# Kernel optimization log

Measured on AMD Instinct MI355X. Metric: run time of the kernel, lower is better.

The kernel has to match this reference:

```python
import jax, jax.numpy as jnp
import numpy as np

D = 128          # feature / hidden dim
K = 3            # SortPooling k (hard-coded in Topkpool)
NUM_CLASS = 10
EPS = 1e-5       # BatchNorm eps


def setup_inputs() -> dict:
    key = jax.random.key(0)
    ks = jax.random.split(key, 24)
    G, NPG = 512, 200
    N = G * NPG
    E = 1638400
    inp = {
        "x": jax.random.normal(ks[0], (N, D), jnp.float32),
        "src": jax.random.randint(ks[1], (E,), 0, N),
        "dst": jax.random.randint(ks[2], (E,), 0, N),
        "num_graphs": G,
        "nodes_per_graph": NPG,
    }
    s = 1.0 / np.sqrt(D)
    for i in (1, 2, 3):
        inp[f"W{i}"] = jax.random.uniform(ks[2 + i], (D, D), jnp.float32, -s, s)
        inp[f"b{i}"] = jnp.zeros((D,), jnp.float32)
        inp[f"g{i}"] = jnp.ones((D,), jnp.float32)   # BN gamma
        inp[f"bt{i}"] = jnp.zeros((D,), jnp.float32)  # BN beta
    sp = 1.0 / np.sqrt(K * D)
    for i in range(4):
        inp[f"P{i}w"] = jax.random.uniform(ks[10 + i], (K * D, NUM_CLASS), jnp.float32, -sp, sp)
        inp[f"P{i}b"] = jnp.zeros((NUM_CLASS,), jnp.float32)
    return inp


def _graph_conv(h, src, dst, W, b, n):
    # DGL GraphConv, norm='both': D_in^{-1/2} A (D_out^{-1/2} h) W + b
    one = jnp.ones((src.shape[0],), h.dtype)
    deg_out = jnp.zeros((n,), h.dtype).at[src].add(one)
    deg_in = jnp.zeros((n,), h.dtype).at[dst].add(one)
    h = h * jax.lax.rsqrt(jnp.maximum(deg_out, 1.0))[:, None]
    agg = jax.ops.segment_sum(h[src], dst, num_segments=n)  # [N, D] scatter-add
    agg = agg * jax.lax.rsqrt(jnp.maximum(deg_in, 1.0))[:, None]
    return agg @ W + b


def _bn_relu(h, g, bt):
    mu = h.mean(axis=0)
    var = jnp.mean((h - mu) ** 2, axis=0)  # biased var, torch BN training mode
    return jax.nn.relu((h - mu) * jax.lax.rsqrt(var + EPS) * g + bt)


def _sort_pool(h, G, npg):
    # DGL SortPooling: sort each node's feature vector ascending, then pick
    # top-K nodes per graph by last (max) channel, concatenate features.
    d = h.shape[-1]
    hs = jnp.sort(h, axis=-1).reshape(G, npg, d)
    idx = jax.lax.top_k(hs[:, :, -1], K)[1]                       # [G, K]
    return jnp.take_along_axis(hs, idx[:, :, None], axis=1).reshape(G, K * d)


def reference(x, W1, b1, g1, bt1, W2, b2, g2, bt2, W3, b3, g3, bt3,
              P0w, P0b, P1w, P1b, P2w, P2b, P3w, P3b,
              src, dst, num_graphs, nodes_per_graph):
    n = x.shape[0]
    reps = [x]
    h = x
    for W, b, g, bt in ((W1, b1, g1, bt1), (W2, b2, g2, bt2), (W3, b3, g3, bt3)):
        h = _bn_relu(_graph_conv(h, src, dst, W, b, n), g, bt)
        reps.append(h)
    score = jnp.zeros((num_graphs, NUM_CLASS), x.dtype)
    for h_i, Pw, Pb in zip(reps, (P0w, P1w, P2w, P3w), (P0b, P1b, P2b, P3b)):
        score = score + _sort_pool(h_i, num_graphs, nodes_per_graph) @ Pw + Pb
    return score
```

## Files before the change

kernel.cpp:

```cpp
#include <hip/hip_runtime.h>
#include <hip/hip_bf16.h>

#define D 128
#define KTOP 3
#define NCLS 10
#define EPS 1e-5f
#define GBM 128
#define BCAP 64


__global__ __launch_bounds__(256) void prologue_kernel(
        const int* __restrict__ src,
        int* __restrict__ deg_out, int E,
        const float* __restrict__ x, float* __restrict__ nodemax, int N,
        float* __restrict__ score, const float* __restrict__ pb0,
        const float* __restrict__ pb1, const float* __restrict__ pb2,
        const float* __restrict__ pb3, int G) {
    int b = blockIdx.x;
    int nbDeg = (E + 255) >> 8;
    if (b < nbDeg) {
        int e = b * 256 + threadIdx.x;
        if (e < E) atomicAdd(&deg_out[src[e]], 1);
        return;
    }
    b -= nbDeg;
    int nbR = N >> 3;
    if (b < nbR) {
        int node = b * 8 + (threadIdx.x >> 5);
        int l = threadIdx.x & 31;
        float4 v = *reinterpret_cast<const float4*>(x + (size_t)node * D + 4 * l);
        float m = fmaxf(fmaxf(v.x, v.y), fmaxf(v.z, v.w));
#pragma unroll
        for (int d = 16; d > 0; d >>= 1) m = fmaxf(m, __shfl_xor(m, d, 64));
        if (l == 0) nodemax[node] = m;
        return;
    }
    for (int i = threadIdx.x; i < G * NCLS; i += 256) {
        int c = i % NCLS;
        score[i] = pb0[c] + pb1[c] + pb2[c] + pb3[c];
    }
}

__global__ void csr_scatter(const int* __restrict__ src, const int* __restrict__ dst,
                            const int* __restrict__ deg_out,
                            int* __restrict__ cursor, int2* __restrict__ csrw, int E) {
    int e = blockIdx.x * blockDim.x + threadIdx.x;
    if (e >= E) return;
    int d = dst[e], s = src[e];
    int slot = atomicAdd(&cursor[d], 1);
    if (slot >= BCAP) return;
    int dg = deg_out[s]; if (dg < 1) dg = 1;
    int2 p; p.x = s; p.y = __float_as_int(rsqrtf((float)dg));
    csrw[(size_t)d * BCAP + slot] = p;
}

__global__ void pad_kernel(const int* __restrict__ cursor, int2* __restrict__ csrw, int N) {
    int d = blockIdx.x * blockDim.x + threadIdx.x;
    if (d >= N) return;
    int c = cursor[d]; if (c > BCAP) c = BCAP;
    int end = (c + 7) & ~7;
    int2 z; z.x = 0; z.y = 0;
    for (int i = c; i < end; ++i) csrw[(size_t)d * BCAP + i] = z;
}

__device__ __forceinline__ float4 bnrelu4(float4 v, float4 sc, float4 sh) {
    float4 r;
    r.x = fmaxf(fmaf(v.x, sc.x, sh.x), 0.f);
    r.y = fmaxf(fmaf(v.y, sc.y, sh.y), 0.f);
    r.z = fmaxf(fmaf(v.z, sc.z, sh.z), 0.f);
    r.w = fmaxf(fmaf(v.w, sc.w, sh.w), 0.f);
    return r;
}


__global__ __launch_bounds__(256) void aggregate_head(
        const float* __restrict__ hin, const int* __restrict__ cursor,
        const int2* __restrict__ csrw, float* __restrict__ hout, int nAgg,
        const float* __restrict__ nodemax, const float* __restrict__ Pw,
        float* __restrict__ score, int NPG,
        const float* __restrict__ bns, const float* __restrict__ g,
        const float* __restrict__ bt, float invN) {
    __shared__ float ov[256];
    __shared__ float sv[256];
    __shared__ int   si[256];
    __shared__ int   sel[KTOP];
    __shared__ float sbuf[KTOP][D];
    __shared__ float red[4][NCLS];
    __shared__ float scs[D], shs[D];
    int b = blockIdx.x;
    int t = threadIdx.x;
    bool useBN = (bns != nullptr);
    if (useBN) {
        if (t < D) {
            float mu  = bns[t] * invN;
            float var = bns[D + t] * invN - mu * mu;
            float inv = rsqrtf(var + EPS);
            float s = g[t] * inv;
            scs[t] = s;
            shs[t] = bt[t] - mu * s;
        }
        __syncthreads();
    }
    if (b < nAgg) {
        int node = b * 8 + (t >> 5);
        int l = t & 31;
        int deg = cursor[node];
        int end = (deg + 7) & ~7; if (end > BCAP) end = BCAP;
        const int2* bkt = csrw + (size_t)node * BCAP;
        const float* base = hin + 4 * l;
        float4 sc4, sh4;
        if (useBN) {
            sc4 = *reinterpret_cast<const float4*>(&scs[4 * l]);
            sh4 = *reinterpret_cast<const float4*>(&shs[4 * l]);
        }
        float4 a0 = {0.f, 0.f, 0.f, 0.f}, a1 = a0;
        for (int e = 0; e < end; e += 8) {
            const int4* ce = reinterpret_cast<const int4*>(bkt + e);
            int4 p0 = ce[0], p1 = ce[1], p2 = ce[2], p3 = ce[3];
            float4 v0 = *reinterpret_cast<const float4*>(base + (size_t)p0.x * D);
            float4 v1 = *reinterpret_cast<const float4*>(base + (size_t)p0.z * D);
            float4 v2 = *reinterpret_cast<const float4*>(base + (size_t)p1.x * D);
            float4 v3 = *reinterpret_cast<const float4*>(base + (size_t)p1.z * D);
            float4 v4 = *reinterpret_cast<const float4*>(base + (size_t)p2.x * D);
            float4 v5 = *reinterpret_cast<const float4*>(base + (size_t)p2.z * D);
            float4 v6 = *reinterpret_cast<const float4*>(base + (size_t)p3.x * D);
            float4 v7 = *reinterpret_cast<const float4*>(base + (size_t)p3.z * D);
            if (useBN) {
                v0 = bnrelu4(v0, sc4, sh4); v1 = bnrelu4(v1, sc4, sh4);
                v2 = bnrelu4(v2, sc4, sh4); v3 = bnrelu4(v3, sc4, sh4);
                v4 = bnrelu4(v4, sc4, sh4); v5 = bnrelu4(v5, sc4, sh4);
                v6 = bnrelu4(v6, sc4, sh4); v7 = bnrelu4(v7, sc4, sh4);
            }
            float w0 = __int_as_float(p0.y), w1 = __int_as_float(p0.w);
            float w2 = __int_as_float(p1.y), w3 = __int_as_float(p1.w);
            float w4 = __int_as_float(p2.y), w5 = __int_as_float(p2.w);
            float w6 = __int_as_float(p3.y), w7 = __int_as_float(p3.w);
            a0.x += w0*v0.x; a0.y += w0*v0.y; a0.z += w0*v0.z; a0.w += w0*v0.w;
            a1.x += w1*v1.x; a1.y += w1*v1.y; a1.z += w1*v1.z; a1.w += w1*v1.w;
            a0.x += w2*v2.x; a0.y += w2*v2.y; a0.z += w2*v2.z; a0.w += w2*v2.w;
            a1.x += w3*v3.x; a1.y += w3*v3.y; a1.z += w3*v3.z; a1.w += w3*v3.w;
            a0.x += w4*v4.x; a0.y += w4*v4.y; a0.z += w4*v4.z; a0.w += w4*v4.w;
            a1.x += w5*v5.x; a1.y += w5*v5.y; a1.z += w5*v5.z; a1.w += w5*v5.w;
            a0.x += w6*v6.x; a0.y += w6*v6.y; a0.z += w6*v6.z; a0.w += w6*v6.w;
            a1.x += w7*v7.x; a1.y += w7*v7.y; a1.z += w7*v7.z; a1.w += w7*v7.w;
        }
        float ri = rsqrtf((float)(deg < 1 ? 1 : deg));
        float4 r;
        r.x = (a0.x + a1.x) * ri;
        r.y = (a0.y + a1.y) * ri;
        r.z = (a0.z + a1.z) * ri;
        r.w = (a0.w + a1.w) * ri;
        *reinterpret_cast<float4*>(hout + (size_t)node * D + 4 * l) = r;
        return;
    }

    int gr = b - nAgg;
    ov[t] = (t < NPG) ? nodemax[(size_t)gr * NPG + t] : -3.4e38f;
    __syncthreads();
    for (int ks = 0; ks < KTOP; ++ks) {
        sv[t] = ov[t]; si[t] = t;
        __syncthreads();
        for (int s = 128; s > 0; s >>= 1) {
            if (t < s) {
                float a = sv[t], c = sv[t + s];
                int ia = si[t], ib = si[t + s];
                if (c > a || (c == a && ib < ia)) { sv[t] = c; si[t] = ib; }
            }
            __syncthreads();
        }
        if (t == 0) { sel[ks] = si[0]; ov[si[0]] = -3.4e38f; }
        __syncthreads();
    }
    int u = t >> 7, tl = t & 127;
    {
        float v = hin[((size_t)gr * NPG + sel[u]) * D + tl];
        sbuf[u][tl] = useBN ? fmaxf(fmaf(v, scs[tl], shs[tl]), 0.f) : v;
        if (t < 128) {
            float v2 = hin[((size_t)gr * NPG + sel[2]) * D + t];
            sbuf[2][t] = useBN ? fmaxf(fmaf(v2, scs[t], shs[t]), 0.f) : v2;
        }
    }
    __syncthreads();
    for (int size = 2; size <= D; size <<= 1) {
        for (int stride = size >> 1; stride > 0; stride >>= 1) {
            int ixj = tl ^ stride;
            if (ixj > tl) {
                float a = sbuf[u][tl], c = sbuf[u][ixj];
                bool up = ((tl & size) == 0);
                if ((a > c) == up) { sbuf[u][tl] = c; sbuf[u][ixj] = a; }
            }
            if (t < 128) {
                int ix2 = t ^ stride;
                if (ix2 > t) {
                    float a = sbuf[2][t], c = sbuf[2][ix2];
                    bool up = ((t & size) == 0);
                    if ((a > c) == up) { sbuf[2][t] = c; sbuf[2][ix2] = a; }
                }
            }
            __syncthreads();
        }
    }
    float part[NCLS];
    float v0 = sbuf[u][tl];
    const float* pw0 = Pw + (size_t)(u * D + tl) * NCLS;
#pragma unroll
    for (int c = 0; c < NCLS; ++c) part[c] = v0 * pw0[c];
    if (t < 128) {
        float v2 = sbuf[2][t];
        const float* pw2 = Pw + (size_t)(2 * D + t) * NCLS;
#pragma unroll
        for (int c = 0; c < NCLS; ++c) part[c] += v2 * pw2[c];
    }
    int lane = t & 63, wid = t >> 6;
#pragma unroll
    for (int c = 0; c < NCLS; ++c) {
        float xx = part[c];
#pragma unroll
        for (int o = 32; o > 0; o >>= 1) xx += __shfl_down(xx, o, 64);
        if (lane == 0) red[wid][c] = xx;
    }
    __syncthreads();
    if (t < NCLS)
        atomicAdd(&score[gr * NCLS + t],
                  red[0][t] + red[1][t] + red[2][t] + red[3][t]);
}


__device__ __forceinline__ void gemm_chunk(const float* __restrict__ ain, size_t rowBase,
        int kc, int c0, const float (*Wl)[D], float (&acc)[4][8]) {
#pragma unroll 2
    for (int k4 = 0; k4 < 16; ++k4) {
        const float* ap = ain + rowBase * D + kc + 4 * k4;
        float4 a0 = *reinterpret_cast<const float4*>(ap);
        float4 a1 = *reinterpret_cast<const float4*>(ap + D);
        float4 a2 = *reinterpret_cast<const float4*>(ap + 2 * D);
        float4 a3 = *reinterpret_cast<const float4*>(ap + 3 * D);
#pragma unroll
        for (int j = 0; j < 4; ++j) {
            int kk = 4 * k4 + j;
            float4 w0 = *reinterpret_cast<const float4*>(&Wl[kk][c0]);
            float4 w1 = *reinterpret_cast<const float4*>(&Wl[kk][c0 + 4]);
            float av[4];
            av[0] = (j==0)?a0.x:(j==1)?a0.y:(j==2)?a0.z:a0.w;
            av[1] = (j==0)?a1.x:(j==1)?a1.y:(j==2)?a1.z:a1.w;
            av[2] = (j==0)?a2.x:(j==1)?a2.y:(j==2)?a2.z:a2.w;
            av[3] = (j==0)?a3.x:(j==1)?a3.y:(j==2)?a3.z:a3.w;
            float wv[8] = {w0.x, w0.y, w0.z, w0.w, w1.x, w1.y, w1.z, w1.w};
#pragma unroll
            for (int i = 0; i < 4; ++i)
#pragma unroll
                for (int jj = 0; jj < 8; ++jj) acc[i][jj] += av[i] * wv[jj];
        }
    }
}

__global__ __launch_bounds__(512) void gemm_bn(const float* __restrict__ ain,
        const float* __restrict__ W, const float* __restrict__ bias,
        float* __restrict__ hout, float* __restrict__ bnsums, int N) {
    __shared__ __align__(16) float Wl[64][D];
    int t = threadIdx.x;
    int cg = t & 15;
    int rs = t >> 4;
    int c0 = cg * 8;
    size_t rowBase = (size_t)blockIdx.x * GBM + 4 * rs;

    float acc[4][8];
#pragma unroll
    for (int i = 0; i < 4; ++i)
#pragma unroll
        for (int j = 0; j < 8; ++j) acc[i][j] = 0.f;

    const float4* Wv = reinterpret_cast<const float4*>(W);
    float4* Wd = reinterpret_cast<float4*>(&Wl[0][0]);
    float4 wpre[4];
#pragma unroll
    for (int i = 0; i < 4; ++i) wpre[i] = Wv[t + 512 * i];
#pragma unroll
    for (int i = 0; i < 4; ++i) Wd[t + 512 * i] = wpre[i];
#pragma unroll
    for (int i = 0; i < 4; ++i) wpre[i] = Wv[2048 + t + 512 * i];
    __syncthreads();
    gemm_chunk(ain, rowBase, 0, c0, Wl, acc);
    __syncthreads();
#pragma unroll
    for (int i = 0; i < 4; ++i) Wd[t + 512 * i] = wpre[i];
    __syncthreads();
    gemm_chunk(ain, rowBase, 64, c0, Wl, acc);

    float4 b0 = *reinterpret_cast<const float4*>(&bias[c0]);
    float4 b1 = *reinterpret_cast<const float4*>(&bias[c0 + 4]);
    float bv[8] = {b0.x, b0.y, b0.z, b0.w, b1.x, b1.y, b1.z, b1.w};
    float cs[8], cq[8];
#pragma unroll
    for (int j = 0; j < 8; ++j) { cs[j] = 0.f; cq[j] = 0.f; }
#pragma unroll
    for (int i = 0; i < 4; ++i) {
#pragma unroll
        for (int j = 0; j < 8; ++j) {
            float v = acc[i][j] + bv[j];
            acc[i][j] = v;
            cs[j] += v;
            cq[j] += v * v;
        }
    }
#pragma unroll
    for (int i = 0; i < 4; ++i) {
        size_t row = rowBase + i;
        float4 o0, o1;
        o0.x = acc[i][0]; o0.y = acc[i][1]; o0.z = acc[i][2]; o0.w = acc[i][3];
        o1.x = acc[i][4]; o1.y = acc[i][5]; o1.z = acc[i][6]; o1.w = acc[i][7];
        *reinterpret_cast<float4*>(&hout[row * D + c0])     = o0;
        *reinterpret_cast<float4*>(&hout[row * D + c0 + 4]) = o1;
    }
#pragma unroll
    for (int j = 0; j < 8; ++j) {
        cs[j] += __shfl_xor(cs[j], 16, 64); cq[j] += __shfl_xor(cq[j], 16, 64);
        cs[j] += __shfl_xor(cs[j], 32, 64); cq[j] += __shfl_xor(cq[j], 32, 64);
    }
    __syncthreads();
    float* red = &Wl[0][0];
    int wid = t >> 6, lane = t & 63;
    if (lane < 16) {
#pragma unroll
        for (int j = 0; j < 8; ++j) {
            red[wid * 256 + lane * 16 + j]     = cs[j];
            red[wid * 256 + lane * 16 + 8 + j] = cq[j];
        }
    }
    __syncthreads();
    if (t < 256) {
        float s = 0.f;
#pragma unroll
        for (int w = 0; w < 8; ++w) s += red[w * 256 + t];
        int cgi = t >> 4, r = t & 15;
        int ch = cgi * 8 + (r & 7);
        atomicAdd(&bnsums[(r < 8 ? 0 : D) + ch], s);
    }
}


__global__ __launch_bounds__(256) void bn_nodemax(const float* __restrict__ h,
        const float* __restrict__ bnsums, const float* __restrict__ g,
        const float* __restrict__ bt, float* __restrict__ nodemax, int N, float invN) {
    __shared__ float sc[D], sh[D];
    int t = threadIdx.x;
    if (t < D) {
        float mu  = bnsums[t] * invN;
        float var = bnsums[D + t] * invN - mu * mu;
        float inv = rsqrtf(var + EPS);
        float s = g[t] * inv;
        sc[t] = s;
        sh[t] = bt[t] - mu * s;
    }
    __syncthreads();
    int node = (blockIdx.x * 256 + t) >> 5;
    int l = t & 31;
    if (node >= N) return;
    float4 v = *reinterpret_cast<const float4*>(h + (size_t)node * D + 4 * l);
    float4 a = *reinterpret_cast<const float4*>(&sc[4 * l]);
    float4 b = *reinterpret_cast<const float4*>(&sh[4 * l]);
    v.x = fmaxf(fmaf(v.x, a.x, b.x), 0.f);
    v.y = fmaxf(fmaf(v.y, a.y, b.y), 0.f);
    v.z = fmaxf(fmaf(v.z, a.z, b.z), 0.f);
    v.w = fmaxf(fmaf(v.w, a.w, b.w), 0.f);
    float m = fmaxf(fmaxf(v.x, v.y), fmaxf(v.z, v.w));
#pragma unroll
    for (int d = 16; d > 0; d >>= 1) m = fmaxf(m, __shfl_xor(m, d, 64));
    if (l == 0) nodemax[node] = m;
}


extern "C" void kernel_launch(void* const* d_in, const int* in_sizes, int n_in,
                              void* d_out, int out_size, void* d_ws, size_t ws_size,
                              hipStream_t stream) {
    const float* x   = (const float*)d_in[0];
    const int*   src = (const int*)d_in[1];
    const int*   dst = (const int*)d_in[2];
    const float* W[3]  = {(const float*)d_in[5],  (const float*)d_in[9],  (const float*)d_in[13]};
    const float* bb[3] = {(const float*)d_in[6],  (const float*)d_in[10], (const float*)d_in[14]};
    const float* gg[3] = {(const float*)d_in[7],  (const float*)d_in[11], (const float*)d_in[15]};
    const float* bt[3] = {(const float*)d_in[8],  (const float*)d_in[12], (const float*)d_in[16]};
    const float* Pw[4] = {(const float*)d_in[17], (const float*)d_in[19], (const float*)d_in[21], (const float*)d_in[23]};
    const float* Pb[4] = {(const float*)d_in[18], (const float*)d_in[20], (const float*)d_in[22], (const float*)d_in[24]};

    int N = in_sizes[0] / D;
    int E = in_sizes[1];
    int G = out_size / NCLS;
    int NPG = N / G;
    float* score = (float*)d_out;

    size_t NF = (size_t)N * D;
    float* fws     = (float*)d_ws;
    float* H       = fws;
    float* T       = H + NF;
    float* nodemax = T + NF;
    float* bnsums  = nodemax + N;
    int* deg_out = (int*)(bnsums + 6 * D);
    int* cursor  = deg_out + N;
    int2* csrw   = (int2*)(cursor + N);

    int nbDeg = (E + 255) >> 8;
    int nbR = N >> 3;
    float invN = 1.0f / (float)N;

    hipMemsetAsync(deg_out, 0, sizeof(int) * (size_t)2 * N, stream);
    hipMemsetAsync(bnsums, 0, sizeof(float) * 6 * D, stream);

    prologue_kernel<<<nbDeg + nbR + 1, 256, 0, stream>>>(
        src, deg_out, E, x, nodemax, N,
        score, Pb[0], Pb[1], Pb[2], Pb[3], G);
    csr_scatter<<<(E + 255) / 256, 256, 0, stream>>>(src, dst, deg_out, cursor, csrw, E);
    pad_kernel<<<(N + 255) / 256, 256, 0, stream>>>(cursor, csrw, N);

    int nAgg = N / 8;
    const float* hin = x;
    const float* curBns = nullptr;
    const float* curG = nullptr;
    const float* curBt = nullptr;
    for (int l = 0; l < 3; ++l) {
        float* bns = bnsums + l * 2 * D;
        aggregate_head<<<nAgg + G, 256, 0, stream>>>(
            hin, cursor, csrw, T, nAgg, nodemax, Pw[l], score, NPG,
            curBns, curG, curBt, invN);
        gemm_bn<<<N / GBM, 512, 0, stream>>>(T, W[l], bb[l], H, bns, N);
        bn_nodemax<<<N / 8, 256, 0, stream>>>(H, bns, gg[l], bt[l], nodemax, N, invN);
        hin = H;
        curBns = bns; curG = gg[l]; curBt = bt[l];
    }
    aggregate_head<<<G, 256, 0, stream>>>(
        H, cursor, csrw, T, 0, nodemax, Pw[3], score, NPG,
        curBns, curG, curBt, invN);
}
```

Before: 833.7 us.

## Partition degree and CSR atomics by XCD node range; prefetch GEMM A tiles

The degree-count and CSR-scatter kernels now launch eight times as many blocks. Blocks are interleaved by XCD (blockIdx & 7), and each block only performs atomics for nodes in its XCD's slice of the node range, so atomic traffic to a given address stays within one XCD's L2. This costs eight reads of the src/dst arrays and many more blocks. Separately, the GEMM inner loop software-prefetches the next A float4 group before computing on the current one.

```diff
diff --git a/kernel.cpp b/kernel.cpp
--- a/kernel.cpp
+++ b/kernel.cpp
@@ -18,12 +18,17 @@
         const float* __restrict__ pb3, int G) {
     int b = blockIdx.x;
     int nbDeg = (E + 255) >> 8;
-    if (b < nbDeg) {
-        int e = b * 256 + threadIdx.x;
-        if (e < E) atomicAdd(&deg_out[src[e]], 1);
+    if (b < 8 * nbDeg) {
+        int xcd = b & 7;
+        int e = (b >> 3) * 256 + threadIdx.x;
+        int lo = xcd * (N >> 3), hi = lo + (N >> 3);
+        if (e < E) {
+            int s = src[e];
+            if (s >= lo && s < hi) atomicAdd(&deg_out[s], 1);
+        }
         return;
     }
-    b -= nbDeg;
+    b -= 8 * nbDeg;
     int nbR = N >> 3;
     if (b < nbR) {
         int node = b * 8 + (threadIdx.x >> 5);
@@ -41,12 +46,19 @@
     }
 }
 
-__global__ void csr_scatter(const int* __restrict__ src, const int* __restrict__ dst,
-                            const int* __restrict__ deg_out,
-                            int* __restrict__ cursor, int2* __restrict__ csrw, int E) {
-    int e = blockIdx.x * blockDim.x + threadIdx.x;
+
+__global__ __launch_bounds__(256) void csr_scatter(
+        const int* __restrict__ src, const int* __restrict__ dst,
+        const int* __restrict__ deg_out,
+        int* __restrict__ cursor, int2* __restrict__ csrw, int E, int N) {
+    int b = blockIdx.x;
+    int xcd = b & 7;
+    int e = (b >> 3) * 256 + threadIdx.x;
     if (e >= E) return;
-    int d = dst[e], s = src[e];
+    int d = dst[e];
+    int lo = xcd * (N >> 3), hi = lo + (N >> 3);
+    if (d < lo || d >= hi) return;
+    int s = src[e];
     int slot = atomicAdd(&cursor[d], 1);
     if (slot >= BCAP) return;
     int dg = deg_out[s]; if (dg < 1) dg = 1;
@@ -228,13 +240,21 @@
 
 __device__ __forceinline__ void gemm_chunk(const float* __restrict__ ain, size_t rowBase,
         int kc, int c0, const float (*Wl)[D], float (&acc)[4][8]) {
+    const float* ap = ain + rowBase * D + kc;
+    float4 a0 = *reinterpret_cast<const float4*>(ap);
+    float4 a1 = *reinterpret_cast<const float4*>(ap + D);
+    float4 a2 = *reinterpret_cast<const float4*>(ap + 2 * D);
+    float4 a3 = *reinterpret_cast<const float4*>(ap + 3 * D);
 #pragma unroll 2
     for (int k4 = 0; k4 < 16; ++k4) {
-        const float* ap = ain + rowBase * D + kc + 4 * k4;
-        float4 a0 = *reinterpret_cast<const float4*>(ap);
-        float4 a1 = *reinterpret_cast<const float4*>(ap + D);
-        float4 a2 = *reinterpret_cast<const float4*>(ap + 2 * D);
-        float4 a3 = *reinterpret_cast<const float4*>(ap + 3 * D);
+        float4 n0 = a0, n1 = a1, n2 = a2, n3 = a3;
+        if (k4 < 15) {
+            const float* np = ap + 4 * (k4 + 1);
+            n0 = *reinterpret_cast<const float4*>(np);
+            n1 = *reinterpret_cast<const float4*>(np + D);
+            n2 = *reinterpret_cast<const float4*>(np + 2 * D);
+            n3 = *reinterpret_cast<const float4*>(np + 3 * D);
+        }
 #pragma unroll
         for (int j = 0; j < 4; ++j) {
             int kk = 4 * k4 + j;
@@ -251,6 +271,7 @@
 #pragma unroll
                 for (int jj = 0; jj < 8; ++jj) acc[i][jj] += av[i] * wv[jj];
         }
+        a0 = n0; a1 = n1; a2 = n2; a3 = n3;
     }
 }
 
@@ -406,10 +427,10 @@
     hipMemsetAsync(deg_out, 0, sizeof(int) * (size_t)2 * N, stream);
     hipMemsetAsync(bnsums, 0, sizeof(float) * 6 * D, stream);
 
-    prologue_kernel<<<nbDeg + nbR + 1, 256, 0, stream>>>(
+    prologue_kernel<<<8 * nbDeg + nbR + 1, 256, 0, stream>>>(
         src, deg_out, E, x, nodemax, N,
         score, Pb[0], Pb[1], Pb[2], Pb[3], G);
-    csr_scatter<<<(E + 255) / 256, 256, 0, stream>>>(src, dst, deg_out, cursor, csrw, E);
+    csr_scatter<<<8 * nbDeg, 256, 0, stream>>>(src, dst, deg_out, cursor, csrw, E, N);
     pad_kernel<<<(N + 255) / 256, 256, 0, stream>>>(cursor, csrw, N);
 
     int nAgg = N / 8;
```

After: 799.3 us, median of 2. 1.04x faster.
